# Performance work log

Hardware: AMD Instinct MI355X
Metric: run time of the kernel (lower is better)

Reference implementation:

```python
import jax, jax.numpy as jnp
import numpy as np

N, DN, DE, DOUT = 100000, 256, 128, 256
M1, B = 32768, 8192
E1, E2 = 10 * M1, 10 * B
DIN = DN + DN + DE  # self feats + (neighbor feats + edge feats)


def setup_inputs() -> dict:
    key = jax.random.key(0)
    ks = jax.random.split(key, 11)
    return {
        "node_features": jax.random.normal(ks[0], (N, DN), dtype=jnp.float32),
        "edge_feats1": jax.random.normal(ks[1], (E1, DE), dtype=jnp.float32),
        "edge_feats2": jax.random.normal(ks[2], (E2, DE), dtype=jnp.float32),
        "W1": jax.random.normal(ks[3], (DOUT, DIN), dtype=jnp.float32),
        "W2": jax.random.normal(ks[4], (DOUT, DIN), dtype=jnp.float32),
        "from_idx1": jax.random.randint(ks[5], (E1,), 0, N),
        "seg_idx1": jax.random.randint(ks[6], (E1,), 0, M1),
        "self_idx1": jax.random.randint(ks[7], (M1,), 0, N),
        "from_idx2": jax.random.randint(ks[8], (E2,), 0, N),
        "seg_idx2": jax.random.randint(ks[9], (E2,), 0, B),
        "self_idx2": jax.random.randint(ks[10], (B,), 0, M1),
    }


def _sage_layer(self_feats, agg_feats, W):
    # combined = cat([self, agg]); out = relu(W @ combined.T).T
    combined = jnp.concatenate([self_feats, agg_feats], axis=1)
    return jax.nn.relu(combined @ W.T)


def reference(node_features, edge_feats1, edge_feats2, W1, W2,
              from_idx1, seg_idx1, self_idx1, from_idx2, seg_idx2, self_idx2):
    m1 = self_idx1.shape[0]
    b = self_idx2.shape[0]
    # layer 1: aggregate over layer-0 -> layer-1 edges
    msg1 = jnp.concatenate([node_features[from_idx1], edge_feats1], axis=1)  # [E1, DN+DE]
    agg1 = jax.ops.segment_sum(msg1, seg_idx1, num_segments=m1)              # [M1, DN+DE]
    h1 = _sage_layer(node_features[self_idx1], agg1, W1)                     # [M1, DOUT]
    # layer 2: aggregate over layer-1 -> batch edges (from_states use raw node feats, as in torch)
    msg2 = jnp.concatenate([node_features[from_idx2], edge_feats2], axis=1)  # [E2, DN+DE]
    agg2 = jax.ops.segment_sum(msg2, seg_idx2, num_segments=b)               # [B, DN+DE]
    h2 = _sage_layer(h1[self_idx2], agg2, W2)                                # [B, DOUT]
    return h2
```

## Files before the change

### kernel.cpp

```cpp
#include <hip/hip_runtime.h>
#include <hip/hip_bf16.h>

#define N_NODES 100000
#define DN      256
#define DE      128
#define DOUT    256
#define M1      32768
#define BSZ     8192
#define E1      327680
#define E2      81920
#define DIN     640
#define DAGG    384
#define WELEMS  (DOUT * DIN)

#define CDIV(a,b) (((a)+(b)-1)/(b))

#define ZERO_INTS (M1 + BSZ + M1 + 64 + 256)
#define S1_ZB 73
#define S1_CB 80
#define S2_MB 8
#define S2_EB 400

typedef __attribute__((ext_vector_type(8))) short bf16x8;
typedef __attribute__((ext_vector_type(4))) float f32x4;
typedef __attribute__((ext_vector_type(2))) float f32x2;
typedef __attribute__((ext_vector_type(4))) unsigned short u16x4;
typedef __attribute__((ext_vector_type(2))) unsigned short u16x2;

__device__ __forceinline__ unsigned short f32_bf16(float f) {
  unsigned u = __float_as_uint(f);
  unsigned r = (u + 0x7FFF + ((u >> 16) & 1)) >> 16;
  return (unsigned short)r;
}


__global__ __launch_bounds__(1024) void setup1_kernel(int* __restrict__ zbase,
                                                      const float* __restrict__ W1,
                                                      const float* __restrict__ W2,
                                                      unsigned short* __restrict__ Wb1,
                                                      unsigned short* __restrict__ Wb2) {
  int b = blockIdx.x, t = threadIdx.x;
  if (b < S1_ZB) {
    int i = b * 1024 + t;
    if (i < ZERO_INTS) zbase[i] = 0;
  } else {
    int i = ((b - S1_ZB) * 1024 + t) * 4;
    const float* s; unsigned short* d; int o;
    if (i < WELEMS) { s = W1; d = Wb1; o = i; }
    else { s = W2; d = Wb2; o = i - WELEMS; }
    f32x4 v = *reinterpret_cast<const f32x4*>(s + o);
    u16x4 r;
    r[0] = f32_bf16(v[0]); r[1] = f32_bf16(v[1]);
    r[2] = f32_bf16(v[2]); r[3] = f32_bf16(v[3]);
    *reinterpret_cast<u16x4*>(d + o) = r;
  }
}


__global__ __launch_bounds__(1024) void setup2_kernel(const int* __restrict__ self2,
                                                      int* __restrict__ claim,
                                                      const int* __restrict__ self1,
                                                      int* __restrict__ remap,
                                                      int* __restrict__ needed,
                                                      int* __restrict__ selfrow1,
                                                      int* __restrict__ nn,
                                                      const int* __restrict__ seg1,
                                                      const int* __restrict__ from1,
                                                      int* __restrict__ cnt1,
                                                      int2* __restrict__ bkt1,
                                                      const int* __restrict__ seg2,
                                                      const int* __restrict__ from2,
                                                      int* __restrict__ cnt2,
                                                      int2* __restrict__ bkt2) {
  int b = blockIdx.x, t = threadIdx.x;
  if (b < S2_MB) {
    int m = self2[b * 1024 + t];
    if (atomicCAS(&claim[m], 0, 1) == 0) {
      int p = atomicAdd(nn, 1);
      remap[m] = p;
      needed[p] = m;
      selfrow1[p] = self1[m];
    }
  } else {
    int e = (b - S2_MB) * 1024 + t;
    if (e < E1) {
      int s = seg1[e];
      int p = atomicAdd(&cnt1[s], 1);
      if (p < 64) bkt1[s * 64 + p] = make_int2(from1[e], e);
    } else {
      int e2 = e - E1;
      int s = seg2[e2];
      int p = atomicAdd(&cnt2[s], 1);
      if (p < 64) bkt2[s * 64 + p] = make_int2(from2[e2], e2);
    }
  }
}


__global__ __launch_bounds__(256) void agg_kernel(const int* __restrict__ needed,
                                                  const int* __restrict__ nn_dev,
                                                  const int* __restrict__ cnt1,
                                                  const int2* __restrict__ bkt1,
                                                  const float* __restrict__ ef1,
                                                  unsigned short* __restrict__ agg1,
                                                  const int* __restrict__ cnt2,
                                                  const int2* __restrict__ bkt2,
                                                  const float* __restrict__ ef2,
                                                  unsigned short* __restrict__ agg2,
                                                  const float* __restrict__ nf,
                                                  const float* __restrict__ zrow) {
  int wv = (blockIdx.x * 256 + threadIdx.x) >> 6;
  int l = threadIdx.x & 63;
  int s0 = wv * 2;
  bool lay1 = s0 < 8192;
  const int2* bkt = lay1 ? bkt1 : bkt2;
  const int* cnt  = lay1 ? cnt1 : cnt2;
  const float* ef = lay1 ? ef1 : ef2;
  unsigned short* aggout = lay1 ? agg1 : agg2;
  int rbase = lay1 ? s0 : s0 - 8192;

  int nnv = lay1 ? *nn_dev : 0;

  int base_[2], nc_[2];
#pragma unroll
  for (int s = 0; s < 2; ++s) {
    int m; bool valid;
    if (lay1) { valid = (s0 + s) < nnv; m = valid ? needed[s0 + s] : 0; }
    else      { valid = true; m = rbase + s; }
    nc_[s] = valid ? min(cnt[m], 64) : 0;
    base_[s] = m * 64;
  }

  int eidp[2], fidp[2];
#pragma unroll
  for (int s = 0; s < 2; ++s) {
    eidp[s] = 0; fidp[s] = 0;
    if (l < nc_[s]) {
      int2 d = bkt[base_[s] + l];
      fidp[s] = d.x; eidp[s] = d.y;
    }
  }

  const float* zra = zrow + l * 4;
  const float* zrb = zrow + l * 2;

  f32x4 accn[2];
  f32x2 accf[2];
#pragma unroll
  for (int s = 0; s < 2; ++s) {
    accn[s] = (f32x4)0.f;
    accf[s] = (f32x2)0.f;
    int nc = nc_[s];
    int eid = eidp[s], fid = fidp[s];
    for (int j = 0; j < nc; j += 8) {
      f32x4 a[8]; f32x2 b[8];
#pragma unroll
      for (int q = 0; q < 8; ++q) {
        int jj = j + q;
        int fq = __shfl(fid, jj & 63);
        int gq = __shfl(eid, jj & 63);
        bool ok = jj < nc;
        const float* pa = ok ? (nf + (size_t)fq * 256 + l * 4) : zra;
        const float* pb = ok ? (ef + (size_t)gq * 128 + l * 2) : zrb;
        a[q] = *reinterpret_cast<const f32x4*>(pa);
        b[q] = *reinterpret_cast<const f32x2*>(pb);
      }
      accn[s] += ((a[0] + a[1]) + (a[2] + a[3])) + ((a[4] + a[5]) + (a[6] + a[7]));
      accf[s] += ((b[0] + b[1]) + (b[2] + b[3])) + ((b[4] + b[5]) + (b[6] + b[7]));
    }
  }

#pragma unroll
  for (int s = 0; s < 2; ++s) {
    unsigned short* orow = aggout + (size_t)(rbase + s) * DAGG;
    u16x4 on;
    on[0] = f32_bf16(accn[s][0]); on[1] = f32_bf16(accn[s][1]);
    on[2] = f32_bf16(accn[s][2]); on[3] = f32_bf16(accn[s][3]);
    *reinterpret_cast<u16x4*>(orow + l * 4) = on;
    u16x2 oe;
    oe[0] = f32_bf16(accf[s][0]); oe[1] = f32_bf16(accf[s][1]);
    *reinterpret_cast<u16x2*>(orow + 256 + l * 2) = oe;
  }
}


template<int MODE>
__global__ __launch_bounds__(256, 4) void gemm_mfma_kernel(const float* __restrict__ tabf,
                                                           const unsigned short* __restrict__ tabb,
                                                           const int* __restrict__ i1,
                                                           const int* __restrict__ i2,
                                                           const unsigned short* __restrict__ agg,
                                                           const unsigned short* __restrict__ Wb,
                                                           float* __restrict__ outf,
                                                           unsigned short* __restrict__ outb,
                                                           const int* __restrict__ nn_dev,
                                                           int nrows_c) {
  const int nrows = nn_dev ? *nn_dev : nrows_c;
  const int row0 = blockIdx.x * 64;
  if (row0 >= nrows) return;
  const int col0 = blockIdx.y * 64;

  __shared__ unsigned short As[64][72];
  __shared__ unsigned short Bs[64][72];

  const int t = threadIdx.x;
  const int lane = t & 63, wid = t >> 6;
  const int wm = wid >> 1, wn = wid & 1;

  const int srow = t >> 2;
  const int scol = (t & 3) * 16;
  const int grow = row0 + srow;
  int ga = -1;
  if (grow < nrows) { int x = i1[grow]; ga = (MODE == 1) ? i2[x] : x; }
  const unsigned short* wrow = Wb + (size_t)(col0 + srow) * DIN + scol;
  const float* tabrow_f = (MODE == 0 && ga >= 0) ? tabf + (size_t)ga * 256 : nullptr;
  const unsigned short* tabrow_b = (MODE == 1 && ga >= 0) ? tabb + (size_t)ga * 256 : nullptr;
  const unsigned short* aggrow = agg + (size_t)grow * DAGG;

  f32x4 acc[2][2];
#pragma unroll
  for (int m = 0; m < 2; ++m)
#pragma unroll
    for (int n = 0; n < 2; ++n) acc[m][n] = (f32x4)0.f;

  bf16x8 ra0, ra1, rb0, rb1;

  auto loadA = [&](int k0, bf16x8& r0, bf16x8& r1) {
    int k = k0 + scol;
    if (ga < 0) { r0 = (bf16x8)(short)0; r1 = (bf16x8)(short)0; return; }
    if (k < 256) {
      if (MODE == 0) {
        const float* s = tabrow_f + k;
        f32x4 x0 = *reinterpret_cast<const f32x4*>(s);
        f32x4 x1 = *reinterpret_cast<const f32x4*>(s + 4);
        f32x4 x2 = *reinterpret_cast<const f32x4*>(s + 8);
        f32x4 x3 = *reinterpret_cast<const f32x4*>(s + 12);
#pragma unroll
        for (int j = 0; j < 4; ++j) {
          r0[j] = (short)f32_bf16(x0[j]); r0[4 + j] = (short)f32_bf16(x1[j]);
          r1[j] = (short)f32_bf16(x2[j]); r1[4 + j] = (short)f32_bf16(x3[j]);
        }
      } else {
        r0 = *reinterpret_cast<const bf16x8*>(tabrow_b + k);
        r1 = *reinterpret_cast<const bf16x8*>(tabrow_b + k + 8);
      }
    } else {
      r0 = *reinterpret_cast<const bf16x8*>(aggrow + (k - 256));
      r1 = *reinterpret_cast<const bf16x8*>(aggrow + (k - 256) + 8);
    }
  };

  loadA(0, ra0, ra1);
  rb0 = *reinterpret_cast<const bf16x8*>(wrow);
  rb1 = *reinterpret_cast<const bf16x8*>(wrow + 8);

  for (int k0 = 0; k0 < DIN; k0 += 64) {
    *reinterpret_cast<bf16x8*>(&As[srow][scol]) = ra0;
    *reinterpret_cast<bf16x8*>(&As[srow][scol + 8]) = ra1;
    *reinterpret_cast<bf16x8*>(&Bs[srow][scol]) = rb0;
    *reinterpret_cast<bf16x8*>(&Bs[srow][scol + 8]) = rb1;
    __syncthreads();

    if (k0 + 64 < DIN) {
      loadA(k0 + 64, ra0, ra1);
      rb0 = *reinterpret_cast<const bf16x8*>(wrow + k0 + 64);
      rb1 = *reinterpret_cast<const bf16x8*>(wrow + k0 + 64 + 8);
    }

#pragma unroll
    for (int ks = 0; ks < 2; ++ks) {
      bf16x8 af[2], bg[2];
#pragma unroll
      for (int m = 0; m < 2; ++m)
        af[m] = *reinterpret_cast<const bf16x8*>(
            &As[wm * 32 + m * 16 + (lane & 15)][ks * 32 + (lane >> 4) * 8]);
#pragma unroll
      for (int n = 0; n < 2; ++n)
        bg[n] = *reinterpret_cast<const bf16x8*>(
            &Bs[wn * 32 + n * 16 + (lane & 15)][ks * 32 + (lane >> 4) * 8]);
#pragma unroll
      for (int m = 0; m < 2; ++m)
#pragma unroll
        for (int n = 0; n < 2; ++n)
          acc[m][n] = __builtin_amdgcn_mfma_f32_16x16x32_bf16(af[m], bg[n], acc[m][n], 0, 0, 0);
    }
    __syncthreads();
  }

  const int rbase = row0 + wm * 32;
  const int cbase = col0 + wn * 32;
#pragma unroll
  for (int m = 0; m < 2; ++m)
#pragma unroll
    for (int n = 0; n < 2; ++n)
#pragma unroll
      for (int g = 0; g < 4; ++g) {
        int r = rbase + m * 16 + (lane >> 4) * 4 + g;
        if (r < nrows) {
          int c = cbase + n * 16 + (lane & 15);
          float x = fmaxf(acc[m][n][g], 0.f);
          if (MODE == 0) outb[(size_t)r * DOUT + c] = f32_bf16(x);
          else outf[(size_t)r * DOUT + c] = x;
        }
      }
}


extern "C" void kernel_launch(void* const* d_in, const int* in_sizes, int n_in,
                              void* d_out, int out_size, void* d_ws, size_t ws_size,
                              hipStream_t stream) {
  const float* nf   = (const float*)d_in[0];
  const float* ef1  = (const float*)d_in[1];
  const float* ef2  = (const float*)d_in[2];
  const float* W1   = (const float*)d_in[3];
  const float* W2   = (const float*)d_in[4];
  const int* from1  = (const int*)d_in[5];
  const int* seg1   = (const int*)d_in[6];
  const int* self1  = (const int*)d_in[7];
  const int* from2  = (const int*)d_in[8];
  const int* seg2   = (const int*)d_in[9];
  const int* self2  = (const int*)d_in[10];
  float* out = (float*)d_out;

  char* w = (char*)d_ws;
  size_t o = 0;
  auto take = [&](size_t nb) -> char* {
    char* p = w + o;
    o += (nb + 255) & ~(size_t)255;
    return p;
  };
  int* cnt1 = (int*)take((size_t)M1 * 4);
  int* cnt2 = (int*)take((size_t)BSZ * 4);
  int* claim = (int*)take((size_t)M1 * 4);
  int* nn   = (int*)take(256);
  float* zrow = (float*)take((size_t)256 * 4);
  int* remap    = (int*)take((size_t)M1 * 4);
  int* needed   = (int*)take((size_t)8192 * 4);
  int* selfrow1 = (int*)take((size_t)8192 * 4);
  int2* bkt1    = (int2*)take((size_t)M1 * 64 * 8);
  int2* bkt2    = (int2*)take((size_t)BSZ * 64 * 8);
  unsigned short* Wb1   = (unsigned short*)take((size_t)WELEMS * 2);
  unsigned short* Wb2   = (unsigned short*)take((size_t)WELEMS * 2);
  unsigned short* agg1c = (unsigned short*)take((size_t)8192 * DAGG * 2);
  unsigned short* agg2  = (unsigned short*)take((size_t)8192 * DAGG * 2);
  unsigned short* h1c   = (unsigned short*)take((size_t)8192 * DOUT * 2);

  setup1_kernel<<<S1_ZB + S1_CB, 1024, 0, stream>>>((int*)d_ws, W1, W2, Wb1, Wb2);
  setup2_kernel<<<S2_MB + S2_EB, 1024, 0, stream>>>(self2, claim, self1, remap, needed,
                                                    selfrow1, nn,
                                                    seg1, from1, cnt1, bkt1,
                                                    seg2, from2, cnt2, bkt2);
  agg_kernel<<<2048, 256, 0, stream>>>(needed, nn, cnt1, bkt1, ef1, agg1c,
                                       cnt2, bkt2, ef2, agg2, nf, zrow);
  gemm_mfma_kernel<0><<<dim3(128, 4), 256, 0, stream>>>(nf, nullptr, selfrow1, nullptr,
                                                        agg1c, Wb1, nullptr, h1c, nn, 0);
  gemm_mfma_kernel<1><<<dim3(128, 4), 256, 0, stream>>>(nullptr, h1c, self2, remap,
                                                        agg2, Wb2, out, nullptr, nullptr, BSZ);
}
```

Measured before the change: 94.55 us.

## Overlap layer-2 aggregation with layer-1 GEMM in one fused launch

Splits the combined aggregation kernel so only layer-1 aggregation runs first. Layer-2 aggregation now runs as extra blocks inside the layer-1 GEMM launch, because it does not depend on h1. The memory-bound gather blocks can then overlap with the MFMA GEMM blocks and fill idle CUs, since the GEMM grid exits early for rows beyond nn. The cost is block heterogeneity: agg blocks inherit the GEMM's launch bounds and shared-memory footprint, which may reduce their occupancy.

```diff
diff --git a/kernel.cpp b/kernel.cpp
--- a/kernel.cpp
+++ b/kernel.cpp
@@ -20,6 +20,7 @@
 #define S1_CB 80
 #define S2_MB 8
 #define S2_EB 400
+#define GEMM1_BLOCKS 512
 
 typedef __attribute__((ext_vector_type(8))) short bf16x8;
 typedef __attribute__((ext_vector_type(4))) float f32x4;
@@ -97,40 +98,22 @@
 }
 
 
-__global__ __launch_bounds__(256) void agg_kernel(const int* __restrict__ needed,
-                                                  const int* __restrict__ nn_dev,
-                                                  const int* __restrict__ cnt1,
-                                                  const int2* __restrict__ bkt1,
-                                                  const float* __restrict__ ef1,
-                                                  unsigned short* __restrict__ agg1,
-                                                  const int* __restrict__ cnt2,
-                                                  const int2* __restrict__ bkt2,
-                                                  const float* __restrict__ ef2,
-                                                  unsigned short* __restrict__ agg2,
-                                                  const float* __restrict__ nf,
-                                                  const float* __restrict__ zrow) {
-  int wv = (blockIdx.x * 256 + threadIdx.x) >> 6;
-  int l = threadIdx.x & 63;
-  int s0 = wv * 2;
-  bool lay1 = s0 < 8192;
-  const int2* bkt = lay1 ? bkt1 : bkt2;
-  const int* cnt  = lay1 ? cnt1 : cnt2;
-  const float* ef = lay1 ? ef1 : ef2;
-  unsigned short* aggout = lay1 ? agg1 : agg2;
-  int rbase = lay1 ? s0 : s0 - 8192;
-
-  int nnv = lay1 ? *nn_dev : 0;
-
+__device__ __forceinline__ void agg_two_segments(int m0, bool v0, int m1, bool v1,
+                                                 int r0, const int* __restrict__ cnt,
+                                                 const int2* __restrict__ bkt,
+                                                 const float* __restrict__ ef,
+                                                 unsigned short* __restrict__ aggout,
+                                                 const float* __restrict__ nf,
+                                                 const float* __restrict__ zrow,
+                                                 int l) {
+  int mm[2] = {m0, m1};
+  bool vv[2] = {v0, v1};
   int base_[2], nc_[2];
 #pragma unroll
   for (int s = 0; s < 2; ++s) {
-    int m; bool valid;
-    if (lay1) { valid = (s0 + s) < nnv; m = valid ? needed[s0 + s] : 0; }
-    else      { valid = true; m = rbase + s; }
-    nc_[s] = valid ? min(cnt[m], 64) : 0;
-    base_[s] = m * 64;
-  }
-
+    nc_[s] = vv[s] ? min(cnt[mm[s]], 64) : 0;
+    base_[s] = mm[s] * 64;
+  }
   int eidp[2], fidp[2];
 #pragma unroll
   for (int s = 0; s < 2; ++s) {
@@ -140,7 +123,6 @@
       fidp[s] = d.x; eidp[s] = d.y;
     }
   }
-
   const float* zra = zrow + l * 4;
   const float* zrb = zrow + l * 2;
 
@@ -172,7 +154,7 @@
 
 #pragma unroll
   for (int s = 0; s < 2; ++s) {
-    unsigned short* orow = aggout + (size_t)(rbase + s) * DAGG;
+    unsigned short* orow = aggout + (size_t)(r0 + s) * DAGG;
     u16x4 on;
     on[0] = f32_bf16(accn[s][0]); on[1] = f32_bf16(accn[s][1]);
     on[2] = f32_bf16(accn[s][2]); on[3] = f32_bf16(accn[s][3]);
@@ -184,21 +166,40 @@
 }
 
 
+__global__ __launch_bounds__(256) void agg1_kernel(const int* __restrict__ needed,
+                                                   const int* __restrict__ nn_dev,
+                                                   const int* __restrict__ cnt1,
+                                                   const int2* __restrict__ bkt1,
+                                                   const float* __restrict__ ef1,
+                                                   unsigned short* __restrict__ agg1,
+                                                   const float* __restrict__ nf,
+                                                   const float* __restrict__ zrow) {
+  int wv = (blockIdx.x * 256 + threadIdx.x) >> 6;
+  int l = threadIdx.x & 63;
+  int s0 = wv * 2;
+  int nnv = *nn_dev;
+  bool v0 = s0 < nnv, v1 = (s0 + 1) < nnv;
+  if (!v0) return;
+  int m0 = needed[s0];
+  int m1 = v1 ? needed[s0 + 1] : 0;
+  agg_two_segments(m0, v0, m1, v1, s0, cnt1, bkt1, ef1, agg1, nf, zrow, l);
+}
+
+
 template<int MODE>
-__global__ __launch_bounds__(256, 4) void gemm_mfma_kernel(const float* __restrict__ tabf,
-                                                           const unsigned short* __restrict__ tabb,
-                                                           const int* __restrict__ i1,
-                                                           const int* __restrict__ i2,
-                                                           const unsigned short* __restrict__ agg,
-                                                           const unsigned short* __restrict__ Wb,
-                                                           float* __restrict__ outf,
-                                                           unsigned short* __restrict__ outb,
-                                                           const int* __restrict__ nn_dev,
-                                                           int nrows_c) {
-  const int nrows = nn_dev ? *nn_dev : nrows_c;
-  const int row0 = blockIdx.x * 64;
+__device__ __forceinline__ void gemm_body(int bx, int by,
+                                          const float* __restrict__ tabf,
+                                          const unsigned short* __restrict__ tabb,
+                                          const int* __restrict__ i1,
+                                          const int* __restrict__ i2,
+                                          const unsigned short* __restrict__ agg,
+                                          const unsigned short* __restrict__ Wb,
+                                          float* __restrict__ outf,
+                                          unsigned short* __restrict__ outb,
+                                          int nrows) {
+  const int row0 = bx * 64;
   if (row0 >= nrows) return;
-  const int col0 = blockIdx.y * 64;
+  const int col0 = by * 64;
 
   __shared__ unsigned short As[64][72];
   __shared__ unsigned short Bs[64][72];
@@ -303,6 +304,42 @@
           else outf[(size_t)r * DOUT + c] = x;
         }
       }
+}
+
+
+__global__ __launch_bounds__(256, 4) void gemm1_agg2_kernel(const float* __restrict__ nf,
+                                                            const int* __restrict__ selfrow1,
+                                                            const unsigned short* __restrict__ agg1,
+                                                            const unsigned short* __restrict__ Wb1,
+                                                            unsigned short* __restrict__ h1c,
+                                                            const int* __restrict__ nn_dev,
+                                                            const int* __restrict__ cnt2,
+                                                            const int2* __restrict__ bkt2,
+                                                            const float* __restrict__ ef2,
+                                                            unsigned short* __restrict__ agg2,
+                                                            const float* __restrict__ zrow) {
+  int b = blockIdx.x;
+  if (b < GEMM1_BLOCKS) {
+    gemm_body<0>(b >> 2, b & 3, nf, nullptr, selfrow1, nullptr, agg1, Wb1,
+                 nullptr, h1c, *nn_dev);
+  } else {
+    int wv = ((b - GEMM1_BLOCKS) * 256 + threadIdx.x) >> 6;
+    int l = threadIdx.x & 63;
+    int s0 = wv * 2;
+    agg_two_segments(s0, true, s0 + 1, true, s0, cnt2, bkt2, ef2, agg2,
+                     nf, zrow, l);
+  }
+}
+
+
+__global__ __launch_bounds__(256, 4) void gemm2_kernel(const unsigned short* __restrict__ h1c,
+                                                       const int* __restrict__ self2,
+                                                       const int* __restrict__ remap,
+                                                       const unsigned short* __restrict__ agg2,
+                                                       const unsigned short* __restrict__ Wb2,
+                                                       float* __restrict__ out) {
+  gemm_body<1>(blockIdx.x, blockIdx.y, nullptr, h1c, self2, remap, agg2, Wb2,
+               out, nullptr, BSZ);
 }
 
 
@@ -350,10 +387,9 @@
                                                     selfrow1, nn,
                                                     seg1, from1, cnt1, bkt1,
                                                     seg2, from2, cnt2, bkt2);
-  agg_kernel<<<2048, 256, 0, stream>>>(needed, nn, cnt1, bkt1, ef1, agg1c,
-                                       cnt2, bkt2, ef2, agg2, nf, zrow);
-  gemm_mfma_kernel<0><<<dim3(128, 4), 256, 0, stream>>>(nf, nullptr, selfrow1, nullptr,
-                                                        agg1c, Wb1, nullptr, h1c, nn, 0);
-  gemm_mfma_kernel<1><<<dim3(128, 4), 256, 0, stream>>>(nullptr, h1c, self2, remap,
-                                                        agg2, Wb2, out, nullptr, nullptr, BSZ);
-}
+  agg1_kernel<<<1024, 256, 0, stream>>>(needed, nn, cnt1, bkt1, ef1, agg1c, nf, zrow);
+  gemm1_agg2_kernel<<<GEMM1_BLOCKS + 1024, 256, 0, stream>>>(nf, selfrow1, agg1c, Wb1,
+                                                             h1c, nn,
+                                                             cnt2, bkt2, ef2, agg2, zrow);
+  gemm2_kernel<<<dim3(128, 4), 256, 0, stream>>>(h1c, self2, remap, agg2, Wb2, out);
+}
```

Result: faster. 90.12 us (-4.7%).
